# Kernel tuning notes

Hardware: AMD Instinct MI355X
Metric: run time of the kernel (lower is better)

## Reference

```python
import jax, jax.numpy as jnp
from jax import lax
import numpy as np

P = 16      # n_latent
T = 16      # n_frames
ALPHA = 0.5


def conv2d(x, w, b):
    # Conv2d(k=3, stride=2, pad=1), NCHW/OIHW
    y = lax.conv_general_dilated(x, w, (2, 2), ((1, 1), (1, 1)),
                                 dimension_numbers=('NCHW', 'OIHW', 'NCHW'))
    return y + b[None, :, None, None]


def convT2d(x, w, b):
    # ConvTranspose2d(k=3, stride=2, pad=1, output_pad=1): lhs_dilation=2,
    # pad low = k-1-p = 1, pad high = k-1-p+op = 2, kernel flipped, I/O swapped.
    wk = jnp.flip(w, (2, 3)).transpose(1, 0, 2, 3)
    y = lax.conv_general_dilated(x, wk, (1, 1), ((1, 2), (1, 2)),
                                 lhs_dilation=(2, 2),
                                 dimension_numbers=('NCHW', 'OIHW', 'NCHW'))
    return y + b[None, :, None, None]


def build_tridiag(D, Boff, alpha):
    # D: [B, P*P*T], Boff: [B, P*P*(T-1)] -> block-tridiagonal [B, P*T, P*T]
    b = D.shape[0]
    Db = D.reshape(b, T, P, P)
    Bb = Boff.reshape(b, T - 1, P, P)
    blocks = jnp.zeros((b, T, T, P, P), D.dtype)
    i = jnp.arange(T)
    blocks = blocks.at[:, i, i].set(Db)                                # diagonal blocks
    blocks = blocks.at[:, i[1:], i[:-1]].set(Bb)                        # sub-diagonal
    blocks = blocks.at[:, i[:-1], i[1:]].set(Bb.transpose(0, 1, 3, 2))  # super-diagonal (transposed)
    M = blocks.transpose(0, 1, 3, 2, 4).reshape(b, P * T, P * T)
    return M + alpha * jnp.eye(P * T, dtype=D.dtype)


def setup_inputs() -> dict:
    key = jax.random.key(0)
    ks = jax.random.split(key, 20)
    B = 256

    def kaiming(k, shape, fan_in):
        return jax.random.normal(k, shape, jnp.float32) * np.float32(np.sqrt(2.0 / fan_in))

    inp = {}
    inp['x'] = jax.random.normal(ks[0], (B, T, 32, 32), jnp.float32)
    inp['eps'] = jax.random.normal(ks[1], (B, P * T), jnp.float32)
    # encoder convs
    inp['w1'] = kaiming(ks[2], (32, 1, 3, 3), 9);     inp['b1'] = jnp.zeros((32,), jnp.float32)
    inp['w2'] = kaiming(ks[3], (32, 32, 3, 3), 288);  inp['b2'] = jnp.zeros((32,), jnp.float32)
    inp['w3'] = kaiming(ks[4], (64, 32, 3, 3), 288);  inp['b3'] = jnp.zeros((64,), jnp.float32)
    inp['w4'] = kaiming(ks[5], (64, 64, 3, 3), 576);  inp['b4'] = jnp.zeros((64,), jnp.float32)
    inp['w5'] = kaiming(ks[6], (64, 64, 3, 3), 576);  inp['b5'] = jnp.zeros((64,), jnp.float32)
    # encoder fc heads
    F = 64 * T
    inp['fc_mu_w'] = kaiming(ks[7], (P * T, F), F);   inp['fc_mu_b'] = jnp.zeros((P * T,), jnp.float32)
    # tiny std so alpha*I dominates -> precision matrix is PD (valid Cholesky)
    inp['fc_D_w'] = jax.random.normal(ks[8], (P * P * T, F), jnp.float32) * np.float32(3e-5)
    inp['fc_D_b'] = jnp.zeros((P * P * T,), jnp.float32)
    inp['fc_B_w'] = jax.random.normal(ks[9], (P * P * (T - 1), F), jnp.float32) * np.float32(3e-5)
    inp['fc_B_b'] = jnp.zeros((P * P * (T - 1),), jnp.float32)
    # decoder
    inp['fc_dec_w'] = kaiming(ks[10], (F, P * T), P * T); inp['fc_dec_b'] = jnp.zeros((F,), jnp.float32)
    inp['wt5'] = kaiming(ks[11], (64, 64, 3, 3), 576); inp['bt5'] = jnp.zeros((64,), jnp.float32)
    inp['wt4'] = kaiming(ks[12], (64, 64, 3, 3), 576); inp['bt4'] = jnp.zeros((64,), jnp.float32)
    inp['wt3'] = kaiming(ks[13], (64, 32, 3, 3), 576); inp['bt3'] = jnp.zeros((32,), jnp.float32)
    inp['wt2'] = kaiming(ks[14], (32, 32, 3, 3), 288); inp['bt2'] = jnp.zeros((32,), jnp.float32)
    inp['wt1'] = kaiming(ks[15], (32, 1, 3, 3), 288);  inp['bt1'] = jnp.zeros((1,), jnp.float32)
    return inp


def reference(x, eps, w1, b1, w2, b2, w3, b3, w4, b4, w5, b5,
              fc_mu_w, fc_mu_b, fc_D_w, fc_D_b, fc_B_w, fc_B_b,
              fc_dec_w, fc_dec_b, wt5, bt5, wt4, bt4, wt3, bt3,
              wt2, bt2, wt1, bt1):
    Bsz = x.shape[0]
    # ---- encode ----
    h = x.reshape(-1, 1, 32, 32)
    for w, b in ((w1, b1), (w2, b2), (w3, b3), (w4, b4), (w5, b5)):
        h = jax.nn.relu(conv2d(h, w, b))      # ends at [B*T, 64, 1, 1]
    h = h.reshape(Bsz, 64 * T)
    mu = h @ fc_mu_w.T + fc_mu_b              # [B, P*T]
    Dv = h @ fc_D_w.T + fc_D_b                # [B, P*P*T]
    Bv = h @ fc_B_w.T + fc_B_b                # [B, P*P*(T-1)]
    # ---- reparametrize ----
    Pm = build_tridiag(Dv, Bv, ALPHA)         # [B, P*T, P*T]
    L = jnp.linalg.cholesky(Pm)               # lower, uses lower triangle (as torch.cholesky)
    cov = jnp.linalg.inv(L)                   # per-sample inverse of Cholesky factor
    z = mu + jnp.einsum('bij,bj->bi', cov, eps)
    # ---- decode ----
    hd = (z @ fc_dec_w.T + fc_dec_b).reshape(-1, 64, 1, 1)
    for w, b in ((wt5, bt5), (wt4, bt4), (wt3, bt3), (wt2, bt2)):
        hd = jax.nn.elu(convT2d(hd, w, b))
    xr = jax.nn.sigmoid(convT2d(hd, wt1, bt1))  # [B*T, 1, 32, 32]
    return (xr, mu, cov, Pm)
```

## Files before the change

kernel.cpp:

```cpp
#include <hip/hip_runtime.h>
#include <cmath>

#define ALPHA 0.5f

__global__ __launch_bounds__(256) void prep_all(
    const float* __restrict__ dw5, const float* __restrict__ dw4,
    const float* __restrict__ dw3, const float* __restrict__ dw2,
    const float* __restrict__ ew2, const float* __restrict__ ew3,
    const float* __restrict__ ew4, const float* __restrict__ ew5,
    float* __restrict__ t5, float* __restrict__ t4,
    float* __restrict__ t3, float* __restrict__ t2,
    float* __restrict__ e2, float* __restrict__ e3,
    float* __restrict__ e4, float* __restrict__ e5,
    float4* __restrict__ Pm4)
{
    const int bid = blockIdx.x;
    if (bid < 16384) {
        Pm4[bid * 256 + threadIdx.x] = make_float4(0.f, 0.f, 0.f, 0.f);
        return;
    }
    int idx = (bid - 16384) * 256 + threadIdx.x;
    if (idx >= 202752) return;
    const float* w; float* t; int CIN, COUT, loc; bool enc = false;
    if (idx < 36864)       { w = dw5; t = t5; CIN = 64; COUT = 64; loc = idx; }
    else if (idx < 73728)  { w = dw4; t = t4; CIN = 64; COUT = 64; loc = idx - 36864; }
    else if (idx < 92160)  { w = dw3; t = t3; CIN = 64; COUT = 32; loc = idx - 73728; }
    else if (idx < 101376) { w = dw2; t = t2; CIN = 32; COUT = 32; loc = idx - 92160; }
    else if (idx < 110592) { w = ew2; t = e2; CIN = 32; COUT = 32; loc = idx - 101376; enc = true; }
    else if (idx < 129024) { w = ew3; t = e3; CIN = 32; COUT = 64; loc = idx - 110592; enc = true; }
    else if (idx < 165888) { w = ew4; t = e4; CIN = 64; COUT = 64; loc = idx - 129024; enc = true; }
    else                   { w = ew5; t = e5; CIN = 64; COUT = 64; loc = idx - 165888; enc = true; }
    int wk = loc % 9; int r = loc / 9; int ci, co;
    if (enc) { ci = r % CIN;  co = r / CIN;  }
    else     { co = r % COUT; ci = r / COUT; }
    t[wk * CIN * COUT + ci * COUT + co] = w[loc];
}

__device__ __forceinline__ int a1map(int iy, int col) {
    return (col & 7)
         | ((iy & 2) << 2)
         | (((iy ^ (iy >> 2)) & 1) << 4)
         | ((col & 8) << 2)
         | ((iy & 4) << 4)
         | ((iy & 8) << 4);
}

__global__ __launch_bounds__(256, 4) void enc_fused(
    const float* __restrict__ x,
    const float* __restrict__ w1,  const float* __restrict__ b1,
    const float* __restrict__ w2t, const float* __restrict__ b2,
    const float* __restrict__ w3t, const float* __restrict__ b3,
    const float* __restrict__ w4t, const float* __restrict__ b4,
    const float* __restrict__ w5t, const float* __restrict__ b5,
    float* __restrict__ hout)
{
    __shared__ __align__(16) float smem[10240];
    float* a1s  = smem;
    float* bse  = smem + 8192;
    float* imgs = bse;
    float* a2s  = bse;
    float* a3s  = smem;
    float* a4s  = smem + 1024;
    float* reds = smem + 1280;

    const int n = blockIdx.x;
    const int tid = threadIdx.x;

    const float* xi = x + n * 1024;
    #pragma unroll
    for (int i = 0; i < 4; i++) {
        int idx = tid + 256 * i;
        int iy = idx >> 5, ix = idx & 31;
        int col = (ix & 1) ? 20 + (ix >> 1) : (ix >> 1);
        imgs[iy * 40 + col] = xi[idx];
    }
    __syncthreads();

    {
        const int oy = tid >> 4, ox = tid & 15;
        float patch[9];
        #pragma unroll
        for (int ky = 0; ky < 3; ky++) {
            const int iy = 2 * oy - 1 + ky;
            #pragma unroll
            for (int kx = 0; kx < 3; kx++) {
                const int ix = 2 * ox - 1 + kx;
                bool v = (iy >= 0) && (ix >= 0);
                int col = (ix & 1) ? 20 + (ix >> 1) : (ix >> 1);
                patch[ky * 3 + kx] = v ? imgs[iy * 40 + col] : 0.f;
            }
        }
        const int ocol = (ox & 1) ? 8 + (ox >> 1) : (ox >> 1);
        const int sidx = a1map(oy, ocol);
        for (int c = 0; c < 32; c++) {
            float acc = b1[c];
            #pragma unroll
            for (int k = 0; k < 9; k++) acc = fmaf(patch[k], w1[c * 9 + k], acc);
            a1s[c * 256 + sidx] = fmaxf(acc, 0.f);
        }
    }
    __syncthreads();

    {
        const int p = tid & 63, oy = p >> 3, ox = p & 7;
        const int c0u = __builtin_amdgcn_readfirstlane(tid >> 6);
        const int cobase = c0u * 8;
        float acc[8];
        #pragma unroll
        for (int r = 0; r < 8; r++) acc[r] = b2[cobase + r];
        int offs[9]; bool val[9];
        #pragma unroll
        for (int ky = 0; ky < 3; ky++) {
            const int iy = 2 * oy - 1 + ky;
            #pragma unroll
            for (int kx = 0; kx < 3; kx++) {
                const int ix = 2 * ox - 1 + kx;
                const bool v = (iy >= 0) && (ix >= 0);
                const int col = (ix & 1) ? 8 + (ix >> 1) : (ix >> 1);
                offs[ky * 3 + kx] = v ? a1map(iy, col) : 0;
                val[ky * 3 + kx] = v;
            }
        }
        for (int ci = 0; ci < 32; ci++) {
            float patch[9];
            #pragma unroll
            for (int k = 0; k < 9; k++)
                patch[k] = val[k] ? a1s[ci * 256 + offs[k]] : 0.f;
            const float* wci = w2t + ci * 32 + cobase;
            #pragma unroll
            for (int k = 0; k < 9; k++) {
                #pragma unroll
                for (int r = 0; r < 8; r++)
                    acc[r] = fmaf(patch[k], wci[k * 1024 + r], acc[r]);
            }
        }
        __syncthreads();
        #pragma unroll
        for (int r = 0; r < 8; r++)
            a2s[(cobase + r) * 64 + p] = fmaxf(acc[r], 0.f);
    }
    __syncthreads();

    {
        const int px = tid & 15, oy = px >> 2, ox = px & 3;
        const int cg = tid >> 4;
        float4 bv = ((const float4*)b3)[cg];
        float acc[4] = {bv.x, bv.y, bv.z, bv.w};
        for (int ci = 0; ci < 32; ci++) {
            float patch[9];
            #pragma unroll
            for (int ky = 0; ky < 3; ky++) {
                const int iy = 2 * oy - 1 + ky;
                #pragma unroll
                for (int kx = 0; kx < 3; kx++) {
                    const int ix = 2 * ox - 1 + kx;
                    bool v = (iy >= 0) && (ix >= 0);
                    patch[ky * 3 + kx] = v ? a2s[ci * 64 + iy * 8 + ix] : 0.f;
                }
            }
            #pragma unroll
            for (int k = 0; k < 9; k++) {
                float4 wv = *(const float4*)(w3t + k * 2048 + ci * 64 + cg * 4);
                acc[0] = fmaf(patch[k], wv.x, acc[0]);
                acc[1] = fmaf(patch[k], wv.y, acc[1]);
                acc[2] = fmaf(patch[k], wv.z, acc[2]);
                acc[3] = fmaf(patch[k], wv.w, acc[3]);
            }
        }
        #pragma unroll
        for (int r = 0; r < 4; r++)
            a3s[(cg * 4 + r) * 16 + px] = fmaxf(acc[r], 0.f);
    }
    __syncthreads();

    {
        const int co = tid & 63;
        const int part = __builtin_amdgcn_readfirstlane(tid >> 6);
        float a0 = 0.f, a1 = 0.f, a2 = 0.f, a3 = 0.f;
        for (int ci = part * 16; ci < part * 16 + 16; ci++) {
            const float* wp = w4t + ci * 64 + co;
            const float w0 = wp[0];
            const float w1 = wp[4096];
            const float w2 = wp[8192];
            const float w3 = wp[12288];
            const float w4 = wp[16384];
            const float w5 = wp[20480];
            const float w6 = wp[24576];
            const float w7 = wp[28672];
            const float w8 = wp[32768];
            const float4 r0 = *(const float4*)(a3s + ci * 16);
            const float4 r1 = *(const float4*)(a3s + ci * 16 + 4);
            const float4 r2 = *(const float4*)(a3s + ci * 16 + 8);
            const float4 r3 = *(const float4*)(a3s + ci * 16 + 12);
            a0 = fmaf(r0.x, w4, a0); a0 = fmaf(r0.y, w5, a0);
            a0 = fmaf(r1.x, w7, a0); a0 = fmaf(r1.y, w8, a0);
            a1 = fmaf(r0.y, w3, a1); a1 = fmaf(r0.z, w4, a1); a1 = fmaf(r0.w, w5, a1);
            a1 = fmaf(r1.y, w6, a1); a1 = fmaf(r1.z, w7, a1); a1 = fmaf(r1.w, w8, a1);
            a2 = fmaf(r1.x, w1, a2); a2 = fmaf(r1.y, w2, a2);
            a2 = fmaf(r2.x, w4, a2); a2 = fmaf(r2.y, w5, a2);
            a2 = fmaf(r3.x, w7, a2); a2 = fmaf(r3.y, w8, a2);
            a3 = fmaf(r1.y, w0, a3); a3 = fmaf(r1.z, w1, a3); a3 = fmaf(r1.w, w2, a3);
            a3 = fmaf(r2.y, w3, a3); a3 = fmaf(r2.z, w4, a3); a3 = fmaf(r2.w, w5, a3);
            a3 = fmaf(r3.y, w6, a3); a3 = fmaf(r3.z, w7, a3); a3 = fmaf(r3.w, w8, a3);
        }
        float* reds2 = bse;
        reds2[part * 256 +   0 + co] = a0;
        reds2[part * 256 +  64 + co] = a1;
        reds2[part * 256 + 128 + co] = a2;
        reds2[part * 256 + 192 + co] = a3;
        __syncthreads();
        {
            const int co2 = tid & 63;
            const int cls2 = __builtin_amdgcn_readfirstlane(tid >> 6);
            float s = b4[co2]
                    + reds2[      cls2 * 64 + co2] + reds2[256 + cls2 * 64 + co2]
                    + reds2[512 + cls2 * 64 + co2] + reds2[768 + cls2 * 64 + co2];
            a4s[co2 * 4 + cls2] = fmaxf(s, 0.f);
        }
    }
    __syncthreads();

    {
        const int c = tid & 63, part = tid >> 6;
        float s = 0.f;
        for (int ci = part * 16; ci < part * 16 + 16; ci++) {
            const float4 av = *(const float4*)(a4s + ci * 4);
            s = fmaf(av.x, w5t[4 * 4096 + ci * 64 + c], s);
            s = fmaf(av.y, w5t[5 * 4096 + ci * 64 + c], s);
            s = fmaf(av.z, w5t[7 * 4096 + ci * 64 + c], s);
            s = fmaf(av.w, w5t[8 * 4096 + ci * 64 + c], s);
        }
        reds[part * 64 + c] = s;
    }
    __syncthreads();
    if (tid < 64) {
        float v = b5[tid] + reds[tid] + reds[64 + tid] + reds[128 + tid] + reds[192 + tid];
        hout[n * 64 + tid] = fmaxf(v, 0.f);
    }
}

__global__ __launch_bounds__(256) void fc_enc(
    const float* __restrict__ h,
    const float* __restrict__ wmu, const float* __restrict__ bmu,
    const float* __restrict__ wD,  const float* __restrict__ bD,
    const float* __restrict__ wB,  const float* __restrict__ bB,
    float* __restrict__ mu, float* __restrict__ Pm)
{
    __shared__ float As[32][65];
    __shared__ float Bs[32][65];
    const int tid = threadIdx.x;
    const int m0 = blockIdx.y * 64;
    const int n0 = blockIdx.x * 64;

    const float* wbase; const float* bias; int nloc; int region;
    if (n0 < 256)       { wbase = wmu; bias = bmu; nloc = n0;        region = 0; }
    else if (n0 < 4352) { wbase = wD;  bias = bD;  nloc = n0 - 256;  region = 1; }
    else                { wbase = wB;  bias = bB;  nloc = n0 - 4352; region = 2; }

    const int tx = tid & 15, ty = tid >> 4;
    float acc[4][4] = {};
    for (int k0 = 0; k0 < 1024; k0 += 32) {
        #pragma unroll
        for (int s = 0; s < 8; s++) {
            int l = tid + 256 * s;
            int row = l >> 5, kk = l & 31;
            As[kk][row] = h[(m0 + row) * 1024 + k0 + kk];
            Bs[kk][row] = wbase[(nloc + row) * 1024 + k0 + kk];
        }
        __syncthreads();
        #pragma unroll
        for (int kk = 0; kk < 32; kk++) {
            float av[4], bv[4];
            #pragma unroll
            for (int i = 0; i < 4; i++) av[i] = As[kk][ty * 4 + i];
            #pragma unroll
            for (int j = 0; j < 4; j++) bv[j] = Bs[kk][tx * 4 + j];
            #pragma unroll
            for (int i = 0; i < 4; i++)
                #pragma unroll
                for (int j = 0; j < 4; j++) acc[i][j] = fmaf(av[i], bv[j], acc[i][j]);
        }
        __syncthreads();
    }
    #pragma unroll
    for (int i = 0; i < 4; i++) {
        int m = m0 + ty * 4 + i;
        size_t pbase = (size_t)m * 65536;
        #pragma unroll
        for (int j = 0; j < 4; j++) {
            int nc = nloc + tx * 4 + j;
            float v = acc[i][j] + bias[nc];
            if (region == 0) {
                mu[m * 256 + nc] = v;
            } else {
                int t = nc >> 8, pi = (nc >> 4) & 15, pj = nc & 15;
                if (region == 1) {
                    int row = t * 16 + pi, col = t * 16 + pj;
                    Pm[pbase + row * 256 + col] = v + (pi == pj ? ALPHA : 0.f);
                } else {
                    int row = (t + 1) * 16 + pi, col = t * 16 + pj;
                    Pm[pbase + row * 256 + col] = v;
                    Pm[pbase + col * 256 + row] = v;
                }
            }
        }
    }
}

__global__ __launch_bounds__(256) void chol_inv(
    const float* __restrict__ Pm, float* __restrict__ cov)
{
    __shared__ __align__(16) float Lb[256 * 32 + 32];
    __shared__ float Ds[4096];
    __shared__ float Bs2[3840];
    const int b = blockIdx.x, tid = threadIdx.x;
    const float* Pb = Pm + (size_t)b * 65536;

    for (int i = tid; i < 8224; i += 256) Lb[i] = 0.f;
    for (int i = tid; i < 4096; i += 256) {
        int t = i >> 8, r = (i >> 4) & 15, c = i & 15;
        Ds[i] = Pb[(t * 16 + r) * 256 + t * 16 + c];
    }
    for (int i = tid; i < 3840; i += 256) {
        int t = i >> 8, r = (i >> 4) & 15, c = i & 15;
        Bs2[i] = Pb[((t + 1) * 16 + r) * 256 + t * 16 + c];
    }
    __syncthreads();

    const int d = tid;
    for (int j = 0; j < 256; j++) {
        const int i = j + d;
        float s = 0.f;
        if (d < 32 && i < 256) {
            int bi = i >> 4, bj = j >> 4, pi = i & 15, pj = j & 15;
            float a;
            if (bi == bj)           a = Ds[bi * 256 + pi * 16 + pj];
            else if (bi == bj + 1)  a = Bs2[bj * 256 + pi * 16 + pj];
            else                    a = 0.f;

            float c[32], p[32];
            const float* cp = Lb + j * 32;
            #pragma unroll
            for (int q = 0; q < 8; q++)
                *(float4*)(c + 4 * q) = *(const float4*)(cp + 4 * q);
            const float* pp = Lb + i * 32 + d;
            #pragma unroll
            for (int m = 1; m < 32; m++) p[m] = pp[m];

            float s0 = 0.f, s1 = 0.f, s2 = 0.f, s3 = 0.f;
            #pragma unroll
            for (int m = 1; m <= 28; m += 4) {
                s0 = fmaf(p[m],     c[m],     s0);
                s1 = fmaf(p[m + 1], c[m + 1], s1);
                s2 = fmaf(p[m + 2], c[m + 2], s2);
                s3 = fmaf(p[m + 3], c[m + 3], s3);
            }
            s0 = fmaf(p[29], c[29], s0);
            s1 = fmaf(p[30], c[30], s1);
            s2 = fmaf(p[31], c[31], s2);
            s = a - ((s0 + s1) + (s2 + s3));
        }
        float diag = __shfl(s, 0);
        float Ljj = sqrtf(diag);
        if (d == 0)                  Lb[j * 32] = Ljj;
        else if (d < 32 && i < 256)  Lb[i * 32 + d] = s / Ljj;
        __syncthreads();
    }

    float* rs = Ds;
    const int j = tid;
    rs[j] = 1.f / Lb[j * 32];
    __syncthreads();

    float* covb = cov + (size_t)b * 65536;
    const int w = __builtin_amdgcn_readfirstlane(j >> 6);
    const int istart = w * 64;

    for (int i = 0; i < istart; i++) covb[i * 256 + j] = 0.f;

    float g[32];
    #pragma unroll
    for (int q = 0; q < 32; q++) g[q] = 0.f;

    for (int c = istart; c < 256; c += 32) {
        #pragma unroll
        for (int u = 0; u < 32; u++) {
            const int i = c + u;
            const float* Lr = Lb + i * 32;
            float lrow[32];
            #pragma unroll
            for (int q = 0; q < 8; q++)
                *(float4*)(lrow + 4 * q) = *(const float4*)(Lr + 4 * q);
            float s0 = 0.f, s1 = 0.f, s2 = 0.f, s3 = 0.f;
            #pragma unroll
            for (int dd = 1; dd < 32; dd += 4) {
                s0 = fmaf(lrow[dd],     g[(u - dd) & 31],     s0);
                if (dd + 1 < 32) s1 = fmaf(lrow[dd + 1], g[(u - dd - 1) & 31], s1);
                if (dd + 2 < 32) s2 = fmaf(lrow[dd + 2], g[(u - dd - 2) & 31], s2);
                if (dd + 3 < 32) s3 = fmaf(lrow[dd + 3], g[(u - dd - 3) & 31], s3);
            }
            float s = (s0 + s1) + (s2 + s3);
            float gi = (((i == j) ? 1.f : 0.f) - s) * rs[i];
            g[u & 31] = gi;
            covb[i * 256 + j] = gi;
        }
    }
}

__global__ __launch_bounds__(256) void zvec_k(
    const float* __restrict__ cov, const float* __restrict__ mu,
    const float* __restrict__ eps, float* __restrict__ z)
{
    __shared__ float es[256];
    const int b = blockIdx.x, i = threadIdx.x;
    es[i] = eps[b * 256 + i];
    __syncthreads();
    const float4* row = (const float4*)(cov + (size_t)b * 65536 + i * 256);
    float s = 0.f;
    #pragma unroll 8
    for (int k = 0; k < 64; k++) {
        float4 v = row[k];
        s = fmaf(v.x, es[4 * k], s);
        s = fmaf(v.y, es[4 * k + 1], s);
        s = fmaf(v.z, es[4 * k + 2], s);
        s = fmaf(v.w, es[4 * k + 3], s);
    }
    z[b * 256 + i] = mu[b * 256 + i] + s;
}

__global__ __launch_bounds__(256) void fc_dec_mu(
    const float* __restrict__ z, const float* __restrict__ w,
    const float* __restrict__ bias, float* __restrict__ hd0,
    const float* __restrict__ h, const float* __restrict__ wmu,
    const float* __restrict__ bmu, float* __restrict__ mu)
{
    __shared__ float sh[1024];
    const int blk = blockIdx.x;
    if (blk < 1024) {
        const int b = blk >> 2;
        const int f = ((blk & 3) << 8) + threadIdx.x;
        sh[threadIdx.x] = z[b * 256 + threadIdx.x];
        __syncthreads();
        const float4* wr = (const float4*)(w + f * 256);
        float s = 0.f;
        #pragma unroll 8
        for (int k = 0; k < 64; k++) {
            float4 v = wr[k];
            s = fmaf(v.x, sh[4 * k], s);
            s = fmaf(v.y, sh[4 * k + 1], s);
            s = fmaf(v.z, sh[4 * k + 2], s);
            s = fmaf(v.w, sh[4 * k + 3], s);
        }
        hd0[b * 1024 + f] = s + bias[f];
    } else {
        const int b = blk - 1024, p = threadIdx.x;
        #pragma unroll
        for (int i = 0; i < 4; i++) sh[p + 256 * i] = h[b * 1024 + p + 256 * i];
        __syncthreads();
        const float4* wr = (const float4*)(wmu + p * 1024);
        float s = 0.f;
        #pragma unroll 8
        for (int k = 0; k < 256; k++) {
            float4 v = wr[k];
            s = fmaf(v.x, sh[4 * k], s);
            s = fmaf(v.y, sh[4 * k + 1], s);
            s = fmaf(v.z, sh[4 * k + 2], s);
            s = fmaf(v.w, sh[4 * k + 3], s);
        }
        mu[b * 256 + p] = s + bmu[p];
    }
}

__device__ __forceinline__ float eluf(float v) { return v > 0.f ? v : expf(v) - 1.f; }

template<int PY, int PX, int HIN, int WIN, class F>
__device__ __forceinline__ void for_taps(int ey, int ex, F&& f) {
    if (PY == 0) {
        if (PX == 0) { f(4, ey, ex, true); }
        else         { f(5, ey, ex, true); f(3, ey, ex + 1, ex + 1 < WIN); }
    } else {
        if (PX == 0) { f(7, ey, ex, true); f(1, ey + 1, ex, ey + 1 < HIN); }
        else {
            f(8, ey, ex, true);
            f(6, ey, ex + 1, ex + 1 < WIN);
            f(2, ey + 1, ex, ey + 1 < HIN);
            f(0, ey + 1, ex + 1, (ey + 1 < HIN) && (ex + 1 < WIN));
        }
    }
}

template<int OY>
__device__ __forceinline__ void t4_row(
    const float* __restrict__ wt4t, const float* __restrict__ bt4,
    const float* __restrict__ d1, float* __restrict__ d2, int co)
{
    float a0 = 0.f, a1 = 0.f, a2 = 0.f, a3 = 0.f;
    const float* wb = wt4t + co;
    for (int ci = 0; ci < 64; ci++) {
        const float* base = d1 + ci * 12;
        if (OY % 2 == 0) {
            float4 r = *(const float4*)(base + (OY / 2) * 4);
            float w10 = wb[3 * 4096 + ci * 64];
            float w11 = wb[4 * 4096 + ci * 64];
            float w12 = wb[5 * 4096 + ci * 64];
            a0 = fmaf(r.x, w11, a0);
            a1 = fmaf(r.x, w12, a1); a1 = fmaf(r.y, w10, a1);
            a2 = fmaf(r.y, w11, a2);
            a3 = fmaf(r.y, w12, a3); a3 = fmaf(r.z, w10, a3);
        } else {
            float4 ra = *(const float4*)(base + ((OY - 1) / 2) * 4);
            float4 rb = *(const float4*)(base + ((OY + 1) / 2) * 4);
            float w20 = wb[6 * 4096 + ci * 64], w21 = wb[7 * 4096 + ci * 64], w22 = wb[8 * 4096 + ci * 64];
            float w00 = wb[0 * 4096 + ci * 64], w01 = wb[1 * 4096 + ci * 64], w02 = wb[2 * 4096 + ci * 64];
            a0 = fmaf(ra.x, w21, a0); a0 = fmaf(rb.x, w01, a0);
            a1 = fmaf(ra.x, w22, a1); a1 = fmaf(ra.y, w20, a1);
            a1 = fmaf(rb.x, w02, a1); a1 = fmaf(rb.y, w00, a1);
            a2 = fmaf(ra.y, w21, a2); a2 = fmaf(rb.y, w01, a2);
            a3 = fmaf(ra.y, w22, a3); a3 = fmaf(ra.z, w20, a3);
            a3 = fmaf(rb.y, w02, a3); a3 = fmaf(rb.z, w00, a3);
        }
    }
    float b = bt4[co];
    float4 o = make_float4(eluf(a0 + b), eluf(a1 + b), eluf(a2 + b), eluf(a3 + b));
    *(float4*)(d2 + co * 44 + OY * 8) = o;
}

template<int M>
__device__ __forceinline__ void xrow(float* acc, const float* R, float w0, float w1, float w2)
{
    #pragma unroll
    for (int m = 0; m < M; m++) {
        acc[2 * m]     = fmaf(R[m], w1, acc[2 * m]);
        acc[2 * m + 1] = fmaf(R[m], w2, acc[2 * m + 1]);
        acc[2 * m + 1] = fmaf(R[m + 1], w0, acc[2 * m + 1]);
    }
}

__global__ __launch_bounds__(256, 4) void dec_fused(
    const float* __restrict__ hd0,
    const float* __restrict__ wt5t, const float* __restrict__ bt5,
    const float* __restrict__ wt4t, const float* __restrict__ bt4,
    const float* __restrict__ wt3t, const float* __restrict__ bt3,
    const float* __restrict__ wt2t, const float* __restrict__ bt2,
    const float* __restrict__ wt1,  const float* __restrict__ bt1,
    float* __restrict__ xr)
{
    __shared__ __align__(16) float smem[9664];
    float* d0  = smem;
    float* d1  = smem + 64;
    float* d2  = smem + 832;
    float* scr = smem + 3648;
    float* d3  = smem + 6208;
    float* d4  = smem;

    const int n = blockIdx.x, tid = threadIdx.x;

    for (int i = tid; i < 3584; i += 256) smem[64 + i] = 0.f;
    for (int i = tid; i < 3456; i += 256) d3[i] = 0.f;
    if (tid < 64) d0[tid] = hd0[n * 64 + tid];
    __syncthreads();

    {
        const int co = tid & 63;
        const int wv = __builtin_amdgcn_readfirstlane(tid >> 6);
        const int oy = wv >> 1, ox = wv & 1;
        const int wk = (oy + 1) * 3 + (ox + 1);
        const float* wp = wt5t + wk * 4096 + co;
        float s = bt5[co];
        for (int ci = 0; ci < 64; ci++)
            s = fmaf(d0[ci], wp[ci * 64], s);
        d1[co * 12 + oy * 4 + ox] = eluf(s);
    }
    __syncthreads();

    {
        const int co = tid & 63;
        const int oyw = __builtin_amdgcn_readfirstlane(tid >> 6);
        if (oyw == 0)      t4_row<0>(wt4t, bt4, d1, d2, co);
        else if (oyw == 1) t4_row<1>(wt4t, bt4, d1, d2, co);
        else if (oyw == 2) t4_row<2>(wt4t, bt4, d1, d2, co);
        else               t4_row<3>(wt4t, bt4, d1, d2, co);
    }
    __syncthreads();

    {
        const int co = tid & 31, pr = (tid >> 5) & 3, cih = tid >> 7;
        const int e = (pr & 1) ? 7 - pr : pr;
        const int o = (pr & 1) ? pr : 7 - pr;
        const int iy_e = e >> 1, iy_o2 = (o - 1) >> 1, iy_o0 = (o + 1) >> 1;
        float acce[8] = {}, acco[8] = {};
        const float* wb = wt3t + co;
        for (int c = 0; c < 32; c++) {
            const int ci = cih * 32 + c;
            const float* base = d2 + ci * 44;
            float re[8], ro2[8], ro0[8];
            *(float4*)(re)      = *(const float4*)(base + iy_e * 8);
            *(float4*)(re + 4)  = *(const float4*)(base + iy_e * 8 + 4);
            *(float4*)(ro2)     = *(const float4*)(base + iy_o2 * 8);
            *(float4*)(ro2 + 4) = *(const float4*)(base + iy_o2 * 8 + 4);
            *(float4*)(ro0)     = *(const float4*)(base + iy_o0 * 8);
            *(float4*)(ro0 + 4) = *(const float4*)(base + iy_o0 * 8 + 4);
            float w10 = wb[3 * 2048 + ci * 32], w11 = wb[4 * 2048 + ci * 32], w12 = wb[5 * 2048 + ci * 32];
            float w20 = wb[6 * 2048 + ci * 32], w21 = wb[7 * 2048 + ci * 32], w22 = wb[8 * 2048 + ci * 32];
            float w00 = wb[0 * 2048 + ci * 32], w01 = wb[1 * 2048 + ci * 32], w02 = wb[2 * 2048 + ci * 32];
            xrow<4>(acce, re, w10, w11, w12);
            xrow<4>(acco, ro2, w20, w21, w22);
            xrow<4>(acco, ro0, w00, w01, w02);
        }
        if (cih == 1) {
            float* s = scr + (tid - 128) * 20;
            #pragma unroll
            for (int k = 0; k < 8; k++) { s[k] = acce[k]; s[8 + k] = acco[k]; }
        }
        __syncthreads();
        if (cih == 0) {
            const float* s = scr + tid * 20;
            const float b = bt3[co];
            float* oe = d3 + co * 108 + e * 12;
            float* oo = d3 + co * 108 + o * 12;
            #pragma unroll
            for (int k = 0; k < 8; k++) {
                oe[k] = eluf(acce[k] + s[k] + b);
                oo[k] = eluf(acco[k] + s[8 + k] + b);
            }
        }
    }
    __syncthreads();

    {
        const int co = tid & 31, org = tid >> 5;
        float acc0[16] = {}, acc1[16] = {};
        const float* wb = wt2t + co;
        for (int ci = 0; ci < 32; ci++) {
            const float* base = d3 + ci * 108 + org * 12;
            float A[12], B[12];
            #pragma unroll
            for (int q = 0; q < 3; q++) {
                *(float4*)(A + 4 * q) = *(const float4*)(base + 4 * q);
                *(float4*)(B + 4 * q) = *(const float4*)(base + 12 + 4 * q);
            }
            float w10 = wb[3 * 1024 + ci * 32], w11 = wb[4 * 1024 + ci * 32], w12 = wb[5 * 1024 + ci * 32];
            float w20 = wb[6 * 1024 + ci * 32], w21 = wb[7 * 1024 + ci * 32], w22 = wb[8 * 1024 + ci * 32];
            float w00 = wb[0 * 1024 + ci * 32], w01 = wb[1 * 1024 + ci * 32], w02 = wb[2 * 1024 + ci * 32];
            xrow<8>(acc0, A, w10, w11, w12);
            xrow<8>(acc1, A, w20, w21, w22);
            xrow<8>(acc1, B, w00, w01, w02);
        }
        __syncthreads();
        const float b = bt2[co];
        float* o0 = d4 + co * 260 + (2 * org) * 16;
        float* o1 = o0 + 16;
        #pragma unroll
        for (int q = 0; q < 4; q++) {
            float4 v0 = make_float4(eluf(acc0[4 * q] + b), eluf(acc0[4 * q + 1] + b),
                                    eluf(acc0[4 * q + 2] + b), eluf(acc0[4 * q + 3] + b));
            float4 v1 = make_float4(eluf(acc1[4 * q] + b), eluf(acc1[4 * q + 1] + b),
                                    eluf(acc1[4 * q + 2] + b), eluf(acc1[4 * q + 3] + b));
            *(float4*)(o0 + 4 * q) = v0;
            *(float4*)(o1 + 4 * q) = v1;
        }
    }
    __syncthreads();

    {
        const int ey = tid >> 4, ex = tid & 15;
        const float bb = bt1[0];
        float* xi = xr + n * 1024;
        float acc[4] = {};
        for (int ci = 0; ci < 32; ci++) {
            const float* a = d4 + ci * 260;
            const float* w = wt1 + ci * 9;
            for_taps<0, 0, 16, 16>(ey, ex, [&](int wk, int iy, int ix, bool v) {
                acc[0] = fmaf(v ? a[iy * 16 + ix] : 0.f, w[wk], acc[0]); });
            for_taps<0, 1, 16, 16>(ey, ex, [&](int wk, int iy, int ix, bool v) {
                acc[1] = fmaf(v ? a[iy * 16 + ix] : 0.f, w[wk], acc[1]); });
            for_taps<1, 0, 16, 16>(ey, ex, [&](int wk, int iy, int ix, bool v) {
                acc[2] = fmaf(v ? a[iy * 16 + ix] : 0.f, w[wk], acc[2]); });
            for_taps<1, 1, 16, 16>(ey, ex, [&](int wk, int iy, int ix, bool v) {
                acc[3] = fmaf(v ? a[iy * 16 + ix] : 0.f, w[wk], acc[3]); });
        }
        xi[(2 * ey) * 32 + 2 * ex]         = 1.f / (1.f + expf(-(acc[0] + bb)));
        xi[(2 * ey) * 32 + 2 * ex + 1]     = 1.f / (1.f + expf(-(acc[1] + bb)));
        xi[(2 * ey + 1) * 32 + 2 * ex]     = 1.f / (1.f + expf(-(acc[2] + bb)));
        xi[(2 * ey + 1) * 32 + 2 * ex + 1] = 1.f / (1.f + expf(-(acc[3] + bb)));
    }
}

extern "C" void kernel_launch(void* const* d_in, const int* in_sizes, int n_in,
                              void* d_out, int out_size, void* d_ws, size_t ws_size,
                              hipStream_t stream)
{
    (void)in_sizes; (void)n_in; (void)out_size; (void)ws_size;
    const float* x    = (const float*)d_in[0];
    const float* eps  = (const float*)d_in[1];
    const float* w1 = (const float*)d_in[2];  const float* b1 = (const float*)d_in[3];
    const float* w2 = (const float*)d_in[4];  const float* b2 = (const float*)d_in[5];
    const float* w3 = (const float*)d_in[6];  const float* b3 = (const float*)d_in[7];
    const float* w4 = (const float*)d_in[8];  const float* b4 = (const float*)d_in[9];
    const float* w5 = (const float*)d_in[10]; const float* b5 = (const float*)d_in[11];
    const float* fc_mu_w = (const float*)d_in[12]; const float* fc_mu_b = (const float*)d_in[13];
    const float* fc_D_w  = (const float*)d_in[14]; const float* fc_D_b  = (const float*)d_in[15];
    const float* fc_B_w  = (const float*)d_in[16]; const float* fc_B_b  = (const float*)d_in[17];
    const float* fc_dec_w = (const float*)d_in[18]; const float* fc_dec_b = (const float*)d_in[19];
    const float* wt5 = (const float*)d_in[20]; const float* bt5 = (const float*)d_in[21];
    const float* wt4 = (const float*)d_in[22]; const float* bt4 = (const float*)d_in[23];
    const float* wt3 = (const float*)d_in[24]; const float* bt3 = (const float*)d_in[25];
    const float* wt2 = (const float*)d_in[26]; const float* bt2 = (const float*)d_in[27];
    const float* wt1 = (const float*)d_in[28]; const float* bt1 = (const float*)d_in[29];

    float* ws   = (float*)d_ws;
    float* h    = ws;
    float* z    = ws + 2359296;
    float* hd0  = ws + 2424832;
    float* wt5t = ws + 2686976;
    float* wt4t = ws + 2723840;
    float* wt3t = ws + 2760704;
    float* wt2t = ws + 2779136;
    float* w2t  = ws + 2788352;
    float* w3t  = ws + 2797568;
    float* w4t  = ws + 2816000;
    float* w5t  = ws + 2852864;

    float* out = (float*)d_out;
    float* xr  = out;
    float* mu  = out + 4194304;
    float* cov = out + 4259840;
    float* Pm  = out + 21037056;

    prep_all<<<17176, 256, 0, stream>>>(wt5, wt4, wt3, wt2, w2, w3, w4, w5,
                                        wt5t, wt4t, wt3t, wt2t, w2t, w3t, w4t, w5t,
                                        (float4*)Pm);
    enc_fused<<<4096, 256, 0, stream>>>(x, w1, b1, w2t, b2, w3t, b3, w4t, b4, w5t, b5, h);
    fc_enc<<<dim3(128, 4), 256, 0, stream>>>(h, fc_mu_w, fc_mu_b, fc_D_w, fc_D_b,
                                             fc_B_w, fc_B_b, mu, Pm);
    chol_inv<<<256, 256, 0, stream>>>(Pm, cov);
    zvec_k<<<256, 256, 0, stream>>>(cov, mu, eps, z);
    fc_dec_mu<<<1280, 256, 0, stream>>>(z, fc_dec_w, fc_dec_b, hd0,
                                        h, fc_mu_w, fc_mu_b, mu);
    dec_fused<<<4096, 256, 0, stream>>>(hd0, wt5t, bt5, wt4t, bt4, wt3t, bt3,
                                        wt2t, bt2, wt1, bt1, xr);
}
```

Before: 955.0 us.

## Shrink encoder LDS footprint, vectorize fc_enc loads, fuse z-vector into Cholesky kernel

The encoder's shared buffer is cut from 10240 to 8192 floats by aliasing stages more tightly, with an extra barrier so the image buffer can be overwritten, and the occupancy hint is raised from 4 to 5 blocks. The fc_enc tile loads become two float4 global loads per operand per thread instead of scalar strided loads. The z = mu + cov·eps product moves into the Cholesky/inverse kernel, dropping a launch and working on the freshly written cov rows while they may still be cached. The extra barrier and the higher occupancy target could raise register pressure or spilling in the encoder, and the z loop reads cov back from global memory.

```diff
diff --git a/kernel.cpp b/kernel.cpp
--- a/kernel.cpp
+++ b/kernel.cpp
@@ -45,7 +45,7 @@
          | ((iy & 8) << 4);
 }
 
-__global__ __launch_bounds__(256, 4) void enc_fused(
+__global__ __launch_bounds__(256, 5) void enc_fused(
     const float* __restrict__ x,
     const float* __restrict__ w1,  const float* __restrict__ b1,
     const float* __restrict__ w2t, const float* __restrict__ b2,
@@ -54,14 +54,14 @@
     const float* __restrict__ w5t, const float* __restrict__ b5,
     float* __restrict__ hout)
 {
-    __shared__ __align__(16) float smem[10240];
-    float* a1s  = smem;
-    float* bse  = smem + 8192;
-    float* imgs = bse;
-    float* a2s  = bse;
-    float* a3s  = smem;
-    float* a4s  = smem + 1024;
-    float* reds = smem + 1280;
+    __shared__ __align__(16) float smem[8192];
+    float* a1s   = smem;
+    float* imgs  = smem;
+    float* a2s   = smem;
+    float* a3s   = smem + 2048;
+    float* a4s   = smem + 3072;
+    float* reds  = smem + 3328;
+    float* reds2 = smem + 3584;
 
     const int n = blockIdx.x;
     const int tid = threadIdx.x;
@@ -90,6 +90,7 @@
                 patch[ky * 3 + kx] = v ? imgs[iy * 40 + col] : 0.f;
             }
         }
+        __syncthreads();
         const int ocol = (ox & 1) ? 8 + (ox >> 1) : (ox >> 1);
         const int sidx = a1map(oy, ocol);
         for (int c = 0; c < 32; c++) {
@@ -203,7 +204,6 @@
             a3 = fmaf(r2.y, w3, a3); a3 = fmaf(r2.z, w4, a3); a3 = fmaf(r2.w, w5, a3);
             a3 = fmaf(r3.y, w6, a3); a3 = fmaf(r3.z, w7, a3); a3 = fmaf(r3.w, w8, a3);
         }
-        float* reds2 = bse;
         reds2[part * 256 +   0 + co] = a0;
         reds2[part * 256 +  64 + co] = a1;
         reds2[part * 256 + 128 + co] = a2;
@@ -258,14 +258,24 @@
     else                { wbase = wB;  bias = bB;  nloc = n0 - 4352; region = 2; }
 
     const int tx = tid & 15, ty = tid >> 4;
+    const int srow = tid >> 2, sq = (tid & 3) * 8;
     float acc[4][4] = {};
     for (int k0 = 0; k0 < 1024; k0 += 32) {
-        #pragma unroll
-        for (int s = 0; s < 8; s++) {
-            int l = tid + 256 * s;
-            int row = l >> 5, kk = l & 31;
-            As[kk][row] = h[(m0 + row) * 1024 + k0 + kk];
-            Bs[kk][row] = wbase[(nloc + row) * 1024 + k0 + kk];
+        {
+            const float* ha = h + (m0 + srow) * 1024 + k0 + sq;
+            const float* wa = wbase + (nloc + srow) * 1024 + k0 + sq;
+            float4 a0 = *(const float4*)(ha);
+            float4 a1 = *(const float4*)(ha + 4);
+            float4 b0 = *(const float4*)(wa);
+            float4 b1 = *(const float4*)(wa + 4);
+            As[sq + 0][srow] = a0.x; As[sq + 1][srow] = a0.y;
+            As[sq + 2][srow] = a0.z; As[sq + 3][srow] = a0.w;
+            As[sq + 4][srow] = a1.x; As[sq + 5][srow] = a1.y;
+            As[sq + 6][srow] = a1.z; As[sq + 7][srow] = a1.w;
+            Bs[sq + 0][srow] = b0.x; Bs[sq + 1][srow] = b0.y;
+            Bs[sq + 2][srow] = b0.z; Bs[sq + 3][srow] = b0.w;
+            Bs[sq + 4][srow] = b1.x; Bs[sq + 5][srow] = b1.y;
+            Bs[sq + 6][srow] = b1.z; Bs[sq + 7][srow] = b1.w;
         }
         __syncthreads();
         #pragma unroll
@@ -307,8 +317,10 @@
     }
 }
 
-__global__ __launch_bounds__(256) void chol_inv(
-    const float* __restrict__ Pm, float* __restrict__ cov)
+__global__ __launch_bounds__(256) void chol_inv_z(
+    const float* __restrict__ Pm, float* __restrict__ cov,
+    const float* __restrict__ mu, const float* __restrict__ eps,
+    float* __restrict__ z)
 {
     __shared__ __align__(16) float Lb[256 * 32 + 32];
     __shared__ float Ds[4096];
@@ -405,27 +417,24 @@
             covb[i * 256 + j] = gi;
         }
     }
-}
-
-__global__ __launch_bounds__(256) void zvec_k(
-    const float* __restrict__ cov, const float* __restrict__ mu,
-    const float* __restrict__ eps, float* __restrict__ z)
-{
-    __shared__ float es[256];
-    const int b = blockIdx.x, i = threadIdx.x;
-    es[i] = eps[b * 256 + i];
-    __syncthreads();
-    const float4* row = (const float4*)(cov + (size_t)b * 65536 + i * 256);
-    float s = 0.f;
-    #pragma unroll 8
-    for (int k = 0; k < 64; k++) {
-        float4 v = row[k];
-        s = fmaf(v.x, es[4 * k], s);
-        s = fmaf(v.y, es[4 * k + 1], s);
-        s = fmaf(v.z, es[4 * k + 2], s);
-        s = fmaf(v.w, es[4 * k + 3], s);
-    }
-    z[b * 256 + i] = mu[b * 256 + i] + s;
+
+    __syncthreads();
+    float* es = Ds + 256;
+    es[tid] = eps[b * 256 + tid];
+    __syncthreads();
+    {
+        const float4* row = (const float4*)(covb + (size_t)tid * 256);
+        float s = 0.f;
+        #pragma unroll 8
+        for (int k = 0; k < 64; k++) {
+            float4 v = row[k];
+            s = fmaf(v.x, es[4 * k], s);
+            s = fmaf(v.y, es[4 * k + 1], s);
+            s = fmaf(v.z, es[4 * k + 2], s);
+            s = fmaf(v.w, es[4 * k + 3], s);
+        }
+        z[b * 256 + tid] = mu[b * 256 + tid] + s;
+    }
 }
 
 __global__ __launch_bounds__(256) void fc_dec_mu(
@@ -733,8 +742,7 @@
     enc_fused<<<4096, 256, 0, stream>>>(x, w1, b1, w2t, b2, w3t, b3, w4t, b4, w5t, b5, h);
     fc_enc<<<dim3(128, 4), 256, 0, stream>>>(h, fc_mu_w, fc_mu_b, fc_D_w, fc_D_b,
                                              fc_B_w, fc_B_b, mu, Pm);
-    chol_inv<<<256, 256, 0, stream>>>(Pm, cov);
-    zvec_k<<<256, 256, 0, stream>>>(cov, mu, eps, z);
+    chol_inv_z<<<256, 256, 0, stream>>>(Pm, cov, mu, eps, z);
     fc_dec_mu<<<1280, 256, 0, stream>>>(z, fc_dec_w, fc_dec_b, hd0,
                                         h, fc_mu_w, fc_mu_b, mu);
     dec_fused<<<4096, 256, 0, stream>>>(hd0, wt5t, bt5, wt4t, bt4, wt3t, bt3,
```

Result: no change. 954.5 us (-0.1%).
